# Kernel tuning notes

Hardware: AMD Instinct MI355X
Metric: run time of the kernel (lower is better)

The kernel has to match this reference:

```python
import jax, jax.numpy as jnp
import numpy as np

N_NODES = 50000
N_EDGES = 800000
DIMX = 64
DIMY = 32
NSMAT = 64
N_MID = 6  # six hidden nsmat->nsmat layers between the input and output projections


def setup_inputs() -> dict:
    key = jax.random.key(0)
    ks = jax.random.split(key, 10)
    node_features = jax.random.normal(ks[0], (N_NODES, DIMX), dtype=jnp.float32)
    edge_index = jax.random.randint(ks[1], (2, N_EDGES), 0, N_NODES, dtype=jnp.int64)
    s_in = 1.0 / np.sqrt(DIMX)
    s_mid = 1.0 / np.sqrt(NSMAT)
    w_in = jax.random.uniform(ks[2], (DIMX, NSMAT), jnp.float32, -s_in, s_in)
    b_in = jax.random.uniform(ks[3], (NSMAT,), jnp.float32, -s_in, s_in)
    w_mid = jax.random.uniform(ks[4], (N_MID, NSMAT, NSMAT), jnp.float32, -s_mid, s_mid)
    b_mid = jax.random.uniform(ks[5], (N_MID, NSMAT), jnp.float32, -s_mid, s_mid)
    w_out = jax.random.uniform(ks[6], (NSMAT, DIMY * DIMX), jnp.float32, -s_mid, s_mid)
    b_out = jax.random.uniform(ks[7], (DIMY * DIMX,), jnp.float32, -s_mid, s_mid)
    return {"node_features": node_features, "edge_index": edge_index,
            "w_in": w_in, "b_in": b_in, "w_mid": w_mid, "b_mid": b_mid,
            "w_out": w_out, "b_out": b_out}


def reference(node_features, edge_index, w_in, b_in, w_mid, b_mid, w_out, b_out):
    # per-node MLP producing a [dimy, dimx] sheaf matrix
    h = jax.nn.relu(node_features @ w_in + b_in)
    for i in range(N_MID):  # fixed small layer count
        h = jax.nn.relu(h @ w_mid[i] + b_mid[i])
    smat = (h @ w_out + b_out).reshape(-1, DIMY, DIMX)  # [N, dimy, dimx]
    # batched matrix-vector transform: q_n = smat_n @ x_n
    q = jnp.einsum('nyx,nx->ny', smat, node_features)  # [N, dimy]
    # LightGCN conv: out_i = sum_{(j->i) in E} q_j / sqrt(deg_j * deg_i)
    row, col = edge_index[0], edge_index[1]
    deg = jax.ops.segment_sum(jnp.ones((N_EDGES,), q.dtype), col, num_segments=N_NODES)
    dinv = jnp.where(deg > 0, jax.lax.rsqrt(jnp.maximum(deg, 1.0)), 0.0)
    norm = dinv[row] * dinv[col]  # [E]
    out = jax.ops.segment_sum(norm[:, None] * q[row], col, num_segments=N_NODES)
    return out
```

## Files before the change

### kernel.cpp

```cpp
#include <hip/hip_runtime.h>
#include <cstddef>

#define N_NODES_C 50000
#define N_NODES_PAD 50048
#define N_EDGES_C 800000
#define CAP 64

typedef _Float16 f16x8 __attribute__((ext_vector_type(8)));
typedef float    f32x4 __attribute__((ext_vector_type(4)));

constexpr int XSTR = 72;
constexpr int MQ_BLOCKS   = 782;
constexpr int DEG_BLOCKS  = 782;

__device__ __forceinline__ void gll16(const void* g, void* l) {
    __builtin_amdgcn_global_load_lds(
        (const __attribute__((address_space(1))) void*)g,
        (__attribute__((address_space(3))) void*)l, 16, 0, 0);
}

__global__ void prep_w_kernel(const float* __restrict__ w_in,
                              const float* __restrict__ w_mid,
                              const float* __restrict__ w_out,
                              _Float16* __restrict__ wT,
                              _Float16* __restrict__ W3T,
                              int* __restrict__ deg)
{
    const int b = blockIdx.x;
    if (b >= 624) {
        const int idx = (b - 624) * 256 + threadIdx.x;
        if (idx < 50048 / 4) {
            int4 z = {0, 0, 0, 0};
            *((int4*)deg + idx) = z;
        }
        return;
    }
    const int idx = b * 256 + threadIdx.x;
    if (idx < 7 * 4096) {
        const int l = idx >> 12, rem = idx & 4095;
        const int k = rem >> 6, j = rem & 63;
        const float v = (l == 0) ? w_in[k * 64 + j]
                                 : w_mid[(size_t)(l - 1) * 4096 + k * 64 + j];
        wT[(size_t)l * 4096 + j * 64 + k] = (_Float16)v;
    } else {
        const int i2 = idx - 7 * 4096;
        const int k = i2 >> 11, r = i2 & 2047;
        const int c = k >> 3;
        const int pos = ((c ^ (r & 7)) << 3) | (k & 7);
        W3T[(size_t)r * 64 + pos] = (_Float16)w_out[(size_t)k * 2048 + r];
    }
}

__launch_bounds__(256, 4)
__global__ void mega_kernel(const float* __restrict__ xf,
                            const float* __restrict__ b_in,
                            const float* __restrict__ b_mid,
                            const _Float16* __restrict__ wT,
                            const _Float16* __restrict__ W3T,
                            const float* __restrict__ b_out,
                            _Float16* __restrict__ qs,
                            const int* __restrict__ row,
                            const int* __restrict__ col,
                            int* __restrict__ deg,
                            unsigned short* __restrict__ src16)
{
    __shared__ _Float16 smem[16896];

    if (blockIdx.x >= MQ_BLOCKS) {
        const int base = (blockIdx.x - MQ_BLOCKS) * 1024 + threadIdx.x;
        #pragma unroll
        for (int u = 0; u < 4; ++u) {
            const int e = base + u * 256;
            if (e < N_EDGES_C) {
                const int c = col[e];
                const int r = atomicAdd(&deg[c], 1);
                src16[(size_t)c * CAP + r] = (unsigned short)row[e];
            }
        }
        return;
    }

    const int t    = threadIdx.x;
    const int w    = t >> 6;
    const int lane = t & 63;
    const int quad = lane >> 4;
    const int lrow = lane & 15;
    const int node0 = blockIdx.x * 64 + w * 16;
    _Float16* hb = &smem[w * 16 * XSTR];

    {
        const int n = min(node0 + lrow, N_NODES_C - 1);
        const float4* src4 = (const float4*)(xf + (size_t)n * 64 + quad * 16);
        _Float16 tmp[16];
        #pragma unroll
        for (int i = 0; i < 4; ++i) {
            const float4 v = src4[i];
            tmp[i * 4 + 0] = (_Float16)v.x;
            tmp[i * 4 + 1] = (_Float16)v.y;
            tmp[i * 4 + 2] = (_Float16)v.z;
            tmp[i * 4 + 3] = (_Float16)v.w;
        }
        *(f16x8*)&hb[lrow * XSTR + quad * 16]     = *(f16x8*)&tmp[0];
        *(f16x8*)&hb[lrow * XSTR + quad * 16 + 8] = *(f16x8*)&tmp[8];
    }

    {
        const _Float16* wTl = wT;
        const float* bsrc = b_in;
        for (int l = 0; l < 7; ++l) {
            const f16x8 A0 = *(const f16x8*)&hb[lrow * XSTR + quad * 8];
            const f16x8 A1 = *(const f16x8*)&hb[lrow * XSTR + 32 + quad * 8];
            #pragma unroll
            for (int Nt = 0; Nt < 4; ++Nt) {
                const f16x8 B0 = *(const f16x8*)(wTl + (Nt * 16 + lrow) * 64 + quad * 8);
                const f16x8 B1 = *(const f16x8*)(wTl + (Nt * 16 + lrow) * 64 + 32 + quad * 8);
                const float bias = bsrc[Nt * 16 + lrow];
                f32x4 C = {0.f, 0.f, 0.f, 0.f};
                C = __builtin_amdgcn_mfma_f32_16x16x32_f16(A0, B0, C, 0, 0, 0);
                C = __builtin_amdgcn_mfma_f32_16x16x32_f16(A1, B1, C, 0, 0, 0);
                #pragma unroll
                for (int r = 0; r < 4; ++r) {
                    const float v = fmaxf(C[r] + bias, 0.f);
                    hb[(quad * 4 + r) * XSTR + Nt * 16 + lrow] = (_Float16)v;
                }
            }
            wTl += 4096;
            bsrc = b_mid + (size_t)l * 64;
        }
    }

    const int ra = node0 + lrow;
    const int na = min(ra, N_NODES_C - 1);

    f16x8 Bha[2];
    #pragma unroll
    for (int ks = 0; ks < 2; ++ks)
        Bha[ks] = *(const f16x8*)&hb[lrow * XSTR + ks * 32 + quad * 8];
    float4 xca[4];
    #pragma unroll
    for (int xt = 0; xt < 4; ++xt)
        xca[xt] = *(const float4*)(xf + (size_t)na * 64 + xt * 16 + quad * 4);

    __syncthreads();

    {
        float* lb = (float*)smem;
        const float* gb = b_out + (size_t)(w * 64 + lane) * 4;
        gll16(gb,        lb + w * 256);
        gll16(gb + 1024, lb + 1024 + w * 256);
        #pragma unroll
        for (int s = 0; s < 2; ++s) {
            _Float16* ld = &smem[4608 + s * 4096 + w * 512];
            const _Float16* gs = W3T + (size_t)s * 4096 + (size_t)(w * 64 + lane) * 8;
            gll16(gs,        ld);
            gll16(gs + 2048, ld + 2048);
        }
    }

    const int swz = lrow & 7;
    const int cp0 = ((quad)     ^ swz) * 8;
    const int cp1 = ((4 + quad) ^ swz) * 8;
    const float* lbf = (const float*)smem;

    int rcur = 0;
    for (int y = 0; y < 32; ++y) {
        if (y == 0)      asm volatile("s_waitcnt vmcnt(2)" ::: "memory");
        else if (y == 1) asm volatile("s_waitcnt vmcnt(3)" ::: "memory");
        else             asm volatile("s_waitcnt vmcnt(4)" ::: "memory");
        __builtin_amdgcn_s_barrier();
        __builtin_amdgcn_sched_barrier(0);

        {
            const int ys = (y + 2) & 31;
            const int ri = (rcur == 0) ? 2 : rcur - 1;
            _Float16* ld = &smem[4608 + ri * 4096 + w * 512];
            const _Float16* gs = W3T + (size_t)ys * 4096 + (size_t)(w * 64 + lane) * 8;
            gll16(gs,        ld);
            gll16(gs + 2048, ld + 2048);
        }

        const _Float16* cur = &smem[4608 + rcur * 4096];
        float qa = 0.f;
        #pragma unroll
        for (int xt = 0; xt < 4; ++xt) {
            const _Float16* rp = cur + (xt * 16 + lrow) * 64;
            const f16x8 A0 = *(const f16x8*)(rp + cp0);
            const f16x8 A1 = *(const f16x8*)(rp + cp1);
            f32x4 Ca = {0.f, 0.f, 0.f, 0.f};
            Ca = __builtin_amdgcn_mfma_f32_16x16x32_f16(A0, Bha[0], Ca, 0, 0, 0);
            Ca = __builtin_amdgcn_mfma_f32_16x16x32_f16(A1, Bha[1], Ca, 0, 0, 0);

            const float4 bf = *(const float4*)(lbf + y * 64 + xt * 16 + quad * 4);
            qa += (Ca[0] + bf.x) * xca[xt].x + (Ca[1] + bf.y) * xca[xt].y
                + (Ca[2] + bf.z) * xca[xt].z + (Ca[3] + bf.w) * xca[xt].w;
        }
        qa += __shfl_xor(qa, 16);
        qa += __shfl_xor(qa, 32);

        if (quad == (y >> 3)) {
            qs[(size_t)ra * 32 + y] = (_Float16)qa;
        }

        rcur = (rcur == 2) ? 0 : rcur + 1;
    }
}

__global__ void gather_kernel(const int* __restrict__ deg,
                              const unsigned short* __restrict__ src16,
                              const _Float16* __restrict__ qs,
                              float* __restrict__ out)
{
    const int t = threadIdx.x;
    const int node = blockIdx.x * 64 + (t >> 2);
    if (node >= N_NODES_C) return;
    const int p = t & 3;
    const int yq = p * 8;
    const int d = deg[node];
    const unsigned short* sp = src16 + (size_t)node * CAP;
    float acc[8] = {0.f, 0.f, 0.f, 0.f, 0.f, 0.f, 0.f, 0.f};
    int s = 0;
    for (; s + 4 <= d; s += 4) {
        const ushort4 r4 = *(const ushort4*)(sp + s);
        const int d0 = deg[r4.x], d1 = deg[r4.y], d2 = deg[r4.z], d3 = deg[r4.w];
        const f16x8 a0 = *(const f16x8*)(qs + (size_t)r4.x * 32 + yq);
        const f16x8 a1 = *(const f16x8*)(qs + (size_t)r4.y * 32 + yq);
        const f16x8 a2 = *(const f16x8*)(qs + (size_t)r4.z * 32 + yq);
        const f16x8 a3 = *(const f16x8*)(qs + (size_t)r4.w * 32 + yq);
        const float v0 = (d0 > 0) ? rsqrtf((float)d0) : 0.f;
        const float v1 = (d1 > 0) ? rsqrtf((float)d1) : 0.f;
        const float v2 = (d2 > 0) ? rsqrtf((float)d2) : 0.f;
        const float v3 = (d3 > 0) ? rsqrtf((float)d3) : 0.f;
        #pragma unroll
        for (int j = 0; j < 8; ++j)
            acc[j] += (float)a0[j] * v0 + (float)a1[j] * v1
                    + (float)a2[j] * v2 + (float)a3[j] * v3;
    }
    for (; s < d; ++s) {
        const int r = sp[s];
        const int dr = deg[r];
        const float vr = (dr > 0) ? rsqrtf((float)dr) : 0.f;
        const f16x8 a = *(const f16x8*)(qs + (size_t)r * 32 + yq);
        #pragma unroll
        for (int j = 0; j < 8; ++j) acc[j] += (float)a[j] * vr;
    }
    const float dv = (d > 0) ? rsqrtf((float)d) : 0.f;
    float4 rA, rB;
    rA.x = acc[0] * dv; rA.y = acc[1] * dv; rA.z = acc[2] * dv; rA.w = acc[3] * dv;
    rB.x = acc[4] * dv; rB.y = acc[5] * dv; rB.z = acc[6] * dv; rB.w = acc[7] * dv;
    *(float4*)(out + (size_t)node * 32 + yq)     = rA;
    *(float4*)(out + (size_t)node * 32 + yq + 4) = rB;
}

extern "C" void kernel_launch(void* const* d_in, const int* in_sizes, int n_in,
                              void* d_out, int out_size, void* d_ws, size_t ws_size,
                              hipStream_t stream)
{
    const float* xf    = (const float*)d_in[0];
    const int*   eidx  = (const int*)d_in[1];
    const float* w_in  = (const float*)d_in[2];
    const float* b_in  = (const float*)d_in[3];
    const float* w_mid = (const float*)d_in[4];
    const float* b_mid = (const float*)d_in[5];
    const float* w_out = (const float*)d_in[6];
    const float* b_out = (const float*)d_in[7];
    float* out = (float*)d_out;

    const int* row = eidx;
    const int* col = eidx + N_EDGES_C;

    char* ws = (char*)d_ws;
    _Float16*       qs    = (_Float16*)(ws + 0);
    int*            deg   = (int*)(ws + 3203072);
    _Float16*       wT    = (_Float16*)(ws + 3403264);
    _Float16*       W3T   = (_Float16*)(ws + 3460608);
    unsigned short* src16 = (unsigned short*)(ws + 3722752);

    prep_w_kernel<<<dim3(624 + 49), dim3(256), 0, stream>>>(
        w_in, w_mid, w_out, wT, W3T, deg);

    mega_kernel<<<dim3(MQ_BLOCKS + DEG_BLOCKS), dim3(256), 0, stream>>>(
        xf, b_in, b_mid, wT, W3T, b_out, qs, row, col, deg, src16);

    gather_kernel<<<dim3(782), dim3(256), 0, stream>>>(deg, src16, qs, out);
}
```

Baseline: 158.5 us.

## Process two output rows per iteration with a four-slot W_out ring buffer

The output-projection loop in mega_kernel now handles two y rows per iteration, so 16 iterations replace 32. The three-slot LDS ring of W_out slices becomes a four-slot ring that prefetches two slices at a time, which halves the number of barriers and waitcnt points and packs the two q results into a single f16x2 store. The cost is more LDS (smem grows from 16896 to 20480 halves), which may lower occupancy against the launch bound of 4 blocks per CU, plus extra register pressure from the doubled accumulators.

```diff
diff --git a/kernel.cpp b/kernel.cpp
--- a/kernel.cpp
+++ b/kernel.cpp
@@ -7,6 +7,7 @@
 #define CAP 64
 
 typedef _Float16 f16x8 __attribute__((ext_vector_type(8)));
+typedef _Float16 f16x2 __attribute__((ext_vector_type(2)));
 typedef float    f32x4 __attribute__((ext_vector_type(4)));
 
 constexpr int XSTR = 72;
@@ -64,7 +65,7 @@
                             int* __restrict__ deg,
                             unsigned short* __restrict__ src16)
 {
-    __shared__ _Float16 smem[16896];
+    __shared__ _Float16 smem[20480];
 
     if (blockIdx.x >= MQ_BLOCKS) {
         const int base = (blockIdx.x - MQ_BLOCKS) * 1024 + threadIdx.x;
@@ -86,7 +87,7 @@
     const int quad = lane >> 4;
     const int lrow = lane & 15;
     const int node0 = blockIdx.x * 64 + w * 16;
-    _Float16* hb = &smem[w * 16 * XSTR];
+    _Float16* hb = &smem[4096 + w * 16 * XSTR];
 
     {
         const int n = min(node0 + lrow, N_NODES_C - 1);
@@ -149,8 +150,8 @@
         gll16(gb,        lb + w * 256);
         gll16(gb + 1024, lb + 1024 + w * 256);
         #pragma unroll
-        for (int s = 0; s < 2; ++s) {
-            _Float16* ld = &smem[4608 + s * 4096 + w * 512];
+        for (int s = 0; s < 4; ++s) {
+            _Float16* ld = &smem[4096 + s * 4096 + w * 512];
             const _Float16* gs = W3T + (size_t)s * 4096 + (size_t)(w * 64 + lane) * 8;
             gll16(gs,        ld);
             gll16(gs + 2048, ld + 2048);
@@ -162,46 +163,63 @@
     const int cp1 = ((4 + quad) ^ swz) * 8;
     const float* lbf = (const float*)smem;
 
-    int rcur = 0;
-    for (int y = 0; y < 32; ++y) {
-        if (y == 0)      asm volatile("s_waitcnt vmcnt(2)" ::: "memory");
-        else if (y == 1) asm volatile("s_waitcnt vmcnt(3)" ::: "memory");
-        else             asm volatile("s_waitcnt vmcnt(4)" ::: "memory");
+    for (int i = 0; i < 16; ++i) {
+        if (i == 0)      asm volatile("s_waitcnt vmcnt(4)" ::: "memory");
+        else if (i == 1) asm volatile("s_waitcnt vmcnt(5)" ::: "memory");
+        else             asm volatile("s_waitcnt vmcnt(1)" ::: "memory");
         __builtin_amdgcn_s_barrier();
         __builtin_amdgcn_sched_barrier(0);
 
-        {
-            const int ys = (y + 2) & 31;
-            const int ri = (rcur == 0) ? 2 : rcur - 1;
-            _Float16* ld = &smem[4608 + ri * 4096 + w * 512];
-            const _Float16* gs = W3T + (size_t)ys * 4096 + (size_t)(w * 64 + lane) * 8;
-            gll16(gs,        ld);
-            gll16(gs + 2048, ld + 2048);
-        }
-
-        const _Float16* cur = &smem[4608 + rcur * 4096];
-        float qa = 0.f;
+        if (i < 15) {
+            const int yn = 2 * i + 2;
+            #pragma unroll
+            for (int q2 = 0; q2 < 2; ++q2) {
+                const int ys = yn + q2;
+                _Float16* ld = &smem[4096 + (ys & 3) * 4096 + w * 512];
+                const _Float16* gs = W3T + (size_t)ys * 4096 + (size_t)(w * 64 + lane) * 8;
+                gll16(gs,        ld);
+                gll16(gs + 2048, ld + 2048);
+            }
+        }
+
+        const int y0 = 2 * i;
+        const int y1 = 2 * i + 1;
+        const _Float16* cur0 = &smem[4096 + (y0 & 3) * 4096];
+        const _Float16* cur1 = &smem[4096 + (y1 & 3) * 4096];
+        float qa0 = 0.f, qa1 = 0.f;
         #pragma unroll
         for (int xt = 0; xt < 4; ++xt) {
-            const _Float16* rp = cur + (xt * 16 + lrow) * 64;
-            const f16x8 A0 = *(const f16x8*)(rp + cp0);
-            const f16x8 A1 = *(const f16x8*)(rp + cp1);
-            f32x4 Ca = {0.f, 0.f, 0.f, 0.f};
-            Ca = __builtin_amdgcn_mfma_f32_16x16x32_f16(A0, Bha[0], Ca, 0, 0, 0);
-            Ca = __builtin_amdgcn_mfma_f32_16x16x32_f16(A1, Bha[1], Ca, 0, 0, 0);
-
-            const float4 bf = *(const float4*)(lbf + y * 64 + xt * 16 + quad * 4);
-            qa += (Ca[0] + bf.x) * xca[xt].x + (Ca[1] + bf.y) * xca[xt].y
-                + (Ca[2] + bf.z) * xca[xt].z + (Ca[3] + bf.w) * xca[xt].w;
-        }
-        qa += __shfl_xor(qa, 16);
-        qa += __shfl_xor(qa, 32);
-
-        if (quad == (y >> 3)) {
-            qs[(size_t)ra * 32 + y] = (_Float16)qa;
-        }
-
-        rcur = (rcur == 2) ? 0 : rcur + 1;
+            const _Float16* rp0 = cur0 + (xt * 16 + lrow) * 64;
+            const _Float16* rp1 = cur1 + (xt * 16 + lrow) * 64;
+            const f16x8 A00 = *(const f16x8*)(rp0 + cp0);
+            const f16x8 A01 = *(const f16x8*)(rp0 + cp1);
+            const f16x8 A10 = *(const f16x8*)(rp1 + cp0);
+            const f16x8 A11 = *(const f16x8*)(rp1 + cp1);
+            f32x4 C0 = {0.f, 0.f, 0.f, 0.f};
+            f32x4 C1 = {0.f, 0.f, 0.f, 0.f};
+            C0 = __builtin_amdgcn_mfma_f32_16x16x32_f16(A00, Bha[0], C0, 0, 0, 0);
+            C0 = __builtin_amdgcn_mfma_f32_16x16x32_f16(A01, Bha[1], C0, 0, 0, 0);
+            C1 = __builtin_amdgcn_mfma_f32_16x16x32_f16(A10, Bha[0], C1, 0, 0, 0);
+            C1 = __builtin_amdgcn_mfma_f32_16x16x32_f16(A11, Bha[1], C1, 0, 0, 0);
+
+            const float4 bf0 = *(const float4*)(lbf + y0 * 64 + xt * 16 + quad * 4);
+            const float4 bf1 = *(const float4*)(lbf + y1 * 64 + xt * 16 + quad * 4);
+            qa0 += (C0[0] + bf0.x) * xca[xt].x + (C0[1] + bf0.y) * xca[xt].y
+                 + (C0[2] + bf0.z) * xca[xt].z + (C0[3] + bf0.w) * xca[xt].w;
+            qa1 += (C1[0] + bf1.x) * xca[xt].x + (C1[1] + bf1.y) * xca[xt].y
+                 + (C1[2] + bf1.z) * xca[xt].z + (C1[3] + bf1.w) * xca[xt].w;
+        }
+        qa0 += __shfl_xor(qa0, 16);
+        qa0 += __shfl_xor(qa0, 32);
+        qa1 += __shfl_xor(qa1, 16);
+        qa1 += __shfl_xor(qa1, 32);
+
+        if (quad == (y0 >> 3)) {
+            f16x2 qp;
+            qp[0] = (_Float16)qa0;
+            qp[1] = (_Float16)qa1;
+            *(f16x2*)&qs[(size_t)ra * 32 + y0] = qp;
+        }
     }
 }
 
```

After: 154.4 us. -2.6%, faster.
